# Kernel optimization log

Hardware: AMD Instinct MI355X
Metric: run time of the kernel (lower is better)

## Reference

```python
import jax, jax.numpy as jnp
import numpy as np

NUM_VNS = 16384
NUM_CNS = 8192
VN_DEG = 3
NUM_EDGES = NUM_VNS * VN_DEG  # 49152
BATCH = 128
NUM_ITER = 8
LLR_MAX = 20.0
PHI_MIN = 8.5e-8      # clip values from _phi
PHI_MAX = 16.635532


def _build_graph():
    # (3,6)-regular Tanner graph, edges listed in variable-node (column) order.
    v = np.repeat(np.arange(NUM_VNS), VN_DEG)          # vn id per edge (sorted)
    j = np.tile(np.arange(VN_DEG), NUM_VNS)
    c = (3 * v + j) % NUM_CNS                          # cn id per edge, no duplicate (v,c) pairs
    perm_cn = np.argsort(c, kind='stable')             # == ind_cn: vn-order -> cn-order
    perm_cn_inv = np.argsort(perm_cn, kind='stable')   # == ind_cn_inv
    cn_ids = c[perm_cn]                                # sorted cn id per edge (cn order)
    return (v.astype(np.int32), cn_ids.astype(np.int32),
            perm_cn.astype(np.int32), perm_cn_inv.astype(np.int32))


def setup_inputs() -> dict:
    key = jax.random.key(0)
    vn_ids, cn_ids, perm_cn, perm_cn_inv = _build_graph()
    llr_ch = 2.0 * jax.random.normal(key, (BATCH, NUM_VNS), dtype=jnp.float32)
    return {
        'llr_ch': llr_ch,
        'vn_ids': jnp.asarray(vn_ids),
        'cn_ids': jnp.asarray(cn_ids),
        'perm_cn': jnp.asarray(perm_cn),
        'perm_cn_inv': jnp.asarray(perm_cn_inv),
    }


def _phi(x):
    # numerically stable helper (Ryan), with the module's clipping
    x = jnp.clip(x, PHI_MIN, PHI_MAX)
    return jnp.log(jnp.exp(x) + 1.0) - jnp.log(jnp.exp(x) - 1.0)


def reference(llr_ch, vn_ids, cn_ids, perm_cn, perm_cn_inv):
    # internal sign convention: logits -> llrs (Sionna multiplies by -1)
    llr = -jnp.clip(llr_ch, -LLR_MAX, LLR_MAX).T       # [num_vns, batch]
    msg0 = jnp.zeros((NUM_EDGES, llr.shape[1]), llr.dtype)

    def body(msg, _):
        # --- variable node update (extrinsic): sum of incoming + channel llr, minus own ---
        vtot = jax.ops.segment_sum(msg, vn_ids, num_segments=NUM_VNS) + llr  # [num_vns, B]
        msg_vn = vtot[vn_ids] - msg                     # [num_edges, B], vn edge order
        # --- permute messages into check-node edge order ---
        m = msg_vn[perm_cn]
        # --- check node update: boxplus-phi ---
        sgn = jnp.where(m < 0, -1.0, 1.0)               # tf.sign with sign(0)->1
        sgn_node = jax.ops.segment_prod(sgn, cn_ids, num_segments=NUM_CNS)
        sgn_ext = jax.lax.stop_gradient(sgn * sgn_node[cn_ids])  # extrinsic sign (+-1)
        mag = _phi(jnp.abs(m))
        mag_sum = jax.ops.segment_sum(mag, cn_ids, num_segments=NUM_CNS)
        msg_cn = sgn_ext * _phi(mag_sum[cn_ids] - mag)  # extrinsic magnitude
        # --- back to variable-node edge order ---
        return msg_cn[perm_cn_inv], None

    msg, _ = jax.lax.scan(body, msg0, None, length=NUM_ITER)
    # marginalize: total llr per vn, then convert back to logits
    x_tot = llr + jax.ops.segment_sum(msg, vn_ids, num_segments=NUM_VNS)
    return -x_tot.T                                     # [batch, num_vns], soft output (hard_out=False)
```

## Files before the change

kernel.cpp:

```cpp
#include <hip/hip_runtime.h>


constexpr int NUM_VNS   = 16384;
constexpr int NUM_CNS   = 8192;
constexpr int NUM_EDGES = 49152;
constexpr int BATCH     = 128;
constexpr int NUM_ITER  = 8;
constexpr float LLR_MAX = 20.0f;
constexpr float PHI_MIN = 8.5e-8f;
constexpr float PHI_MAX = 16.635532f;

__device__ __forceinline__ double lean_exp(double x) {
    double t = x * 1.4426950408889634;
    double k = __builtin_rint(t);
    double r = __builtin_fma(-k, 0.6931471805599453, x);
    r = __builtin_fma(-k, 2.3190468138462996e-17, r);
    double p = 1.0 / 3628800.0;
    p = __builtin_fma(p, r, 1.0 / 362880.0);
    p = __builtin_fma(p, r, 1.0 / 40320.0);
    p = __builtin_fma(p, r, 1.0 / 5040.0);
    p = __builtin_fma(p, r, 1.0 / 720.0);
    p = __builtin_fma(p, r, 1.0 / 120.0);
    p = __builtin_fma(p, r, 1.0 / 24.0);
    p = __builtin_fma(p, r, 1.0 / 6.0);
    p = __builtin_fma(p, r, 0.5);
    p = __builtin_fma(p, r, 1.0);
    p = __builtin_fma(p, r, 1.0);
    int ik = (int)k;
    double s = __hiloint2double((1023 + ik) << 20, 0);
    return p * s;
}

__device__ __forceinline__ double lean_log(double v) {
    int hv = __double2hiint(v);
    int lv = __double2loint(v);
    int e  = (hv >> 20) - 1023;
    double m = __hiloint2double((hv & 0x000FFFFF) | 0x3FF00000, lv);
    if (m >= 1.4142135623730951) { m *= 0.5; e += 1; }
    double t = m - 1.0;
    double d = t + 2.0;
    double r = (double)__builtin_amdgcn_rcpf((float)d);
    r = __builtin_fma(__builtin_fma(-d, r, 1.0), r, r);
    double u = t * r;
    double w = u * u;
    double P = 2.0 / 13.0;
    P = __builtin_fma(P, w, 2.0 / 11.0);
    P = __builtin_fma(P, w, 2.0 / 9.0);
    P = __builtin_fma(P, w, 2.0 / 7.0);
    P = __builtin_fma(P, w, 2.0 / 5.0);
    P = __builtin_fma(P, w, 2.0 / 3.0);
    P = __builtin_fma(P, w, 2.0);
    double lm = u * P;
    return __builtin_fma((double)e, 0.6931471805599453, lm);
}

__device__ __forceinline__ float phi_f(float xf) {
    xf = fminf(fmaxf(xf, PHI_MIN), PHI_MAX);
    float exf = (float)lean_exp((double)xf);
    float af = exf + 1.0f;
    float bf = exf - 1.0f;
    float la = (float)lean_log((double)af);
    float lb = (float)lean_log((double)bf);
    return la - lb;
}

constexpr double EXP_STEP = 0.0027076061740622864;
constexpr double EXP_INV  = 369.32993046757465;

__device__ __forceinline__ double fast_exp(double x, const double* et) {
    double kd = __builtin_rint(x * EXP_INV);
    double r  = __builtin_fma(-kd, EXP_STEP, x);
    int n = (int)kd;
    double p = __builtin_fma(r, __builtin_fma(r, 0.5, 1.0), 1.0);
    double s = et[n & 255];
    int sh = __double2hiint(s) + ((n >> 8) << 20);
    s = __hiloint2double(sh, __double2loint(s));
    return p * s;
}

__device__ __forceinline__ double fast_log(double v, const double2* lt) {
    int hv = __double2hiint(v);
    int lv = __double2loint(v);
    int E  = (hv >> 20) - 1023;
    double m = __hiloint2double((hv & 0x000FFFFF) | 0x3FF00000, lv);
    int idx = (hv >> 12) & 255;
    double2 te = lt[idx];
    double t = __hiloint2double(0x3FF00000 | (idx << 12), 0);
    double d = m - t;
    double f = d * te.x;
    double P = __builtin_fma(f, 1.0 / 3.0, -0.5);
    double q = __builtin_fma(f * f, P, f);
    return __builtin_fma((double)E, 0.6931471805599453, te.y + q);
}

__device__ __forceinline__ float phi_fast(float xf, const double2* lt,
                                          const double* et) {
    xf = fminf(fmaxf(xf, PHI_MIN), PHI_MAX);
    float exf = (float)fast_exp((double)xf, et);
    float af = exf + 1.0f;
    float bf = exf - 1.0f;
    float la = (float)fast_log((double)af, lt);
    float lb = (float)fast_log((double)bf, lt);
    return la - lb;
}

template<int FIRST>
__global__ __launch_bounds__(256)
void cn_fused(const float* __restrict__ llr, const float* __restrict__ msgIn,
              float* __restrict__ msgOut)
{
    __shared__ double2 lt[256];
    __shared__ double  et[256];
    {
        int tid = threadIdx.x;
        {
            double t = 1.0 + tid * 0.00390625;
            double r0 = (double)__builtin_amdgcn_rcpf((float)t);
            r0 = __builtin_fma(__builtin_fma(-t, r0, 1.0), r0, r0);
            r0 = __builtin_fma(__builtin_fma(-t, r0, 1.0), r0, r0);
            lt[tid] = make_double2(r0, lean_log(t));
        }
        et[tid] = lean_exp(tid * EXP_STEP);
    }
    __syncthreads();

    int bid = blockIdx.x;
    int seq = bid >> 3;
    int b   = (bid & 7) * 16 + (seq >> 5);
    int c   = (seq & 31) * 256 + threadIdx.x;

    const float* mi = msgIn + (size_t)b * NUM_EDGES;
    float* mo = msgOut + (size_t)b * NUM_EDGES;
    const float* lbp = llr + (size_t)b * NUM_VNS;

    float g[6];
#pragma unroll
    for (int t = 0; t < 6; ++t) {
        int e = c + (t << 13);
        int v = (int)(((unsigned)e * 43691u) >> 17);
        float x = fminf(fmaxf(lbp[v], -LLR_MAX), LLR_MAX);
        float m;
        if (FIRST) {
            m = -x;
        } else {
            int e0 = 3 * v;
            int j  = e - e0;
            float m0 = mi[e0], m1 = mi[e0 + 1], m2 = mi[e0 + 2];
            float s = ((m0 + m1) + m2) - x;
            float own = (j == 0) ? m0 : ((j == 1) ? m1 : m2);
            m = s - own;
        }
        unsigned neg = (m < 0.0f) ? 0x80000000u : 0u;
        float mg = phi_fast(fabsf(m), lt, et);
        g[t] = __uint_as_float(__float_as_uint(mg) | neg);
    }
    float a0 = fabsf(g[0]), a1 = fabsf(g[1]), a2 = fabsf(g[2]);
    float a3 = fabsf(g[3]), a4 = fabsf(g[4]), a5 = fabsf(g[5]);
    float ms = ((((a0 + a1) + a2) + a3) + a4) + a5;
    unsigned all6 = (__float_as_uint(g[0]) ^ __float_as_uint(g[1])
                   ^ __float_as_uint(g[2]) ^ __float_as_uint(g[3])
                   ^ __float_as_uint(g[4]) ^ __float_as_uint(g[5]))
                  & 0x80000000u;
#pragma unroll
    for (int t = 0; t < 6; ++t) {
        int e = c + (t << 13);
        float o = phi_fast(ms - fabsf(g[t]), lt, et);
        unsigned sg = all6 ^ (__float_as_uint(g[t]) & 0x80000000u);
        mo[e] = __uint_as_float(__float_as_uint(o) ^ sg);
    }
}

__global__ __launch_bounds__(256)
void vn_final(const float* __restrict__ llr, const float* __restrict__ msg,
              float* __restrict__ outv)
{
    int bid = blockIdx.x;
    int seq = bid >> 3;
    int b   = (bid & 7) * 16 + (seq >> 6);
    int v   = (seq & 63) * 256 + threadIdx.x;
    float x = fminf(fmaxf(llr[(size_t)b * NUM_VNS + v], -LLR_MAX), LLR_MAX);
    const float* mb = msg + (size_t)b * NUM_EDGES;
    int e = 3 * v;
    float s = ((mb[e] + mb[e + 1]) + mb[e + 2]) - x;
    outv[(size_t)b * NUM_VNS + v] = -s;
}

template<int FIRST, int LAST>
__global__ __launch_bounds__(256)
void vn_kernel(const float* __restrict__ llr, const float* __restrict__ msg,
               float* __restrict__ outv)
{
    int gid = blockIdx.x * 256 + threadIdx.x;
    int b = gid >> 14;
    int v = gid & 16383;
    float x = fminf(fmaxf(llr[gid], -LLR_MAX), LLR_MAX);
    float s;
    if (FIRST) {
        s = -x;
    } else {
        const float* mb = msg + (size_t)b * NUM_EDGES;
        int e = 3 * v;
        s = ((mb[e] + mb[e + 1]) + mb[e + 2]) - x;
    }
    outv[gid] = LAST ? -s : s;
}

template<int FIRST>
__global__ __launch_bounds__(256)
void cn_kernel(float* __restrict__ msg, const float* __restrict__ vtot)
{
    int gid = blockIdx.x * 256 + threadIdx.x;
    int b = gid >> 13;
    int c = gid & 8191;
    float* mb = msg + (size_t)b * NUM_EDGES;
    const float* vt = vtot + (size_t)b * NUM_VNS;

    float g[6];
#pragma unroll
    for (int t = 0; t < 6; ++t) {
        int e = c + (t << 13);
        int v = (int)(((unsigned)e * 43691u) >> 17);
        float m = FIRST ? vt[v] : (vt[v] - mb[e]);
        unsigned neg = (m < 0.0f) ? 0x80000000u : 0u;
        float mg = phi_f(fabsf(m));
        g[t] = __uint_as_float(__float_as_uint(mg) | neg);
    }
    float a0 = fabsf(g[0]), a1 = fabsf(g[1]), a2 = fabsf(g[2]);
    float a3 = fabsf(g[3]), a4 = fabsf(g[4]), a5 = fabsf(g[5]);
    float ms = ((((a0 + a1) + a2) + a3) + a4) + a5;
    unsigned all6 = (__float_as_uint(g[0]) ^ __float_as_uint(g[1])
                   ^ __float_as_uint(g[2]) ^ __float_as_uint(g[3])
                   ^ __float_as_uint(g[4]) ^ __float_as_uint(g[5]))
                  & 0x80000000u;
#pragma unroll
    for (int t = 0; t < 6; ++t) {
        int e = c + (t << 13);
        float o = phi_f(ms - fabsf(g[t]));
        unsigned sg = all6 ^ (__float_as_uint(g[t]) & 0x80000000u);
        mb[e] = __uint_as_float(__float_as_uint(o) ^ sg);
    }
}

extern "C" void kernel_launch(void* const* d_in, const int* in_sizes, int n_in,
                              void* d_out, int out_size, void* d_ws, size_t ws_size,
                              hipStream_t stream) {
    const float* llr = (const float*)d_in[0];
    float* out = (float*)d_out;

    const int VNB = BATCH * NUM_VNS / 256;
    const int CNB = BATCH * NUM_CNS / 256;
    const size_t MSGSZ = (size_t)BATCH * NUM_EDGES;

    if (ws_size >= 2 * MSGSZ * sizeof(float)) {
        float* buf0 = (float*)d_ws;
        float* buf1 = buf0 + MSGSZ;
        cn_fused<1><<<CNB, 256, 0, stream>>>(llr, buf0, buf0);
        for (int it = 1; it < NUM_ITER; ++it) {
            float* in  = (it & 1) ? buf0 : buf1;
            float* dst = (it & 1) ? buf1 : buf0;
            cn_fused<0><<<CNB, 256, 0, stream>>>(llr, in, dst);
        }
        vn_final<<<VNB, 256, 0, stream>>>(llr, buf1, out);
    } else {
        float* msg  = (float*)d_ws;
        float* vtot = msg + MSGSZ;
        vn_kernel<1, 0><<<VNB, 256, 0, stream>>>(llr, msg, vtot);
        cn_kernel<1><<<CNB, 256, 0, stream>>>(msg, vtot);
        for (int it = 1; it < NUM_ITER; ++it) {
            vn_kernel<0, 0><<<VNB, 256, 0, stream>>>(llr, msg, vtot);
            cn_kernel<0><<<CNB, 256, 0, stream>>>(msg, vtot);
        }
        vn_kernel<0, 1><<<VNB, 256, 0, stream>>>(llr, msg, out);
    }
}
```

Baseline: 203.8 us.

## Fuse final VN marginalization into last CN kernel via atomics; two CNs per thread

Each thread now processes two check nodes, halving the grid so the per-block shared-memory table setup is amortized over twice the work. The last iteration's check-node kernel scatters its outgoing messages straight into the output with atomicAdd, with the channel LLR added once per variable node. This removes the separate vn_final kernel and one full message write plus read, at the cost of a memset and float atomics whose summation order is nondeterministic.

Measured after the change: 410.1 us. +101.3%, slower.

```diff
diff --git a/kernel.cpp b/kernel.cpp
--- a/kernel.cpp
+++ b/kernel.cpp
@@ -104,85 +104,86 @@
     return la - lb;
 }
 
-template<int FIRST>
+template<int FIRST, int LAST>
 __global__ __launch_bounds__(256)
-void cn_fused(const float* __restrict__ llr, const float* __restrict__ msgIn,
-              float* __restrict__ msgOut)
+void cn_fused2(const float* __restrict__ llr, const float* __restrict__ msgIn,
+               float* __restrict__ msgOut, float* __restrict__ outv)
 {
     __shared__ double2 lt[256];
     __shared__ double  et[256];
     {
         int tid = threadIdx.x;
-        {
-            double t = 1.0 + tid * 0.00390625;
-            double r0 = (double)__builtin_amdgcn_rcpf((float)t);
-            r0 = __builtin_fma(__builtin_fma(-t, r0, 1.0), r0, r0);
-            r0 = __builtin_fma(__builtin_fma(-t, r0, 1.0), r0, r0);
-            lt[tid] = make_double2(r0, lean_log(t));
-        }
+        double t = 1.0 + tid * 0.00390625;
+        double r0 = (double)__builtin_amdgcn_rcpf((float)t);
+        r0 = __builtin_fma(__builtin_fma(-t, r0, 1.0), r0, r0);
+        r0 = __builtin_fma(__builtin_fma(-t, r0, 1.0), r0, r0);
+        lt[tid] = make_double2(r0, lean_log(t));
         et[tid] = lean_exp(tid * EXP_STEP);
     }
     __syncthreads();
 
     int bid = blockIdx.x;
     int seq = bid >> 3;
-    int b   = (bid & 7) * 16 + (seq >> 5);
-    int c   = (seq & 31) * 256 + threadIdx.x;
+    int b   = (bid & 7) * 16 + (seq >> 4);
+    int ch  = (seq & 15) * 256 + threadIdx.x;
 
     const float* mi = msgIn + (size_t)b * NUM_EDGES;
     float* mo = msgOut + (size_t)b * NUM_EDGES;
     const float* lbp = llr + (size_t)b * NUM_VNS;
-
-    float g[6];
-#pragma unroll
-    for (int t = 0; t < 6; ++t) {
-        int e = c + (t << 13);
-        int v = (int)(((unsigned)e * 43691u) >> 17);
-        float x = fminf(fmaxf(lbp[v], -LLR_MAX), LLR_MAX);
-        float m;
-        if (FIRST) {
-            m = -x;
-        } else {
-            int e0 = 3 * v;
-            int j  = e - e0;
-            float m0 = mi[e0], m1 = mi[e0 + 1], m2 = mi[e0 + 2];
-            float s = ((m0 + m1) + m2) - x;
-            float own = (j == 0) ? m0 : ((j == 1) ? m1 : m2);
-            m = s - own;
-        }
-        unsigned neg = (m < 0.0f) ? 0x80000000u : 0u;
-        float mg = phi_fast(fabsf(m), lt, et);
-        g[t] = __uint_as_float(__float_as_uint(mg) | neg);
-    }
-    float a0 = fabsf(g[0]), a1 = fabsf(g[1]), a2 = fabsf(g[2]);
-    float a3 = fabsf(g[3]), a4 = fabsf(g[4]), a5 = fabsf(g[5]);
-    float ms = ((((a0 + a1) + a2) + a3) + a4) + a5;
-    unsigned all6 = (__float_as_uint(g[0]) ^ __float_as_uint(g[1])
-                   ^ __float_as_uint(g[2]) ^ __float_as_uint(g[3])
-                   ^ __float_as_uint(g[4]) ^ __float_as_uint(g[5]))
-                  & 0x80000000u;
-#pragma unroll
-    for (int t = 0; t < 6; ++t) {
-        int e = c + (t << 13);
-        float o = phi_fast(ms - fabsf(g[t]), lt, et);
-        unsigned sg = all6 ^ (__float_as_uint(g[t]) & 0x80000000u);
-        mo[e] = __uint_as_float(__float_as_uint(o) ^ sg);
-    }
-}
-
-__global__ __launch_bounds__(256)
-void vn_final(const float* __restrict__ llr, const float* __restrict__ msg,
-              float* __restrict__ outv)
-{
-    int bid = blockIdx.x;
-    int seq = bid >> 3;
-    int b   = (bid & 7) * 16 + (seq >> 6);
-    int v   = (seq & 63) * 256 + threadIdx.x;
-    float x = fminf(fmaxf(llr[(size_t)b * NUM_VNS + v], -LLR_MAX), LLR_MAX);
-    const float* mb = msg + (size_t)b * NUM_EDGES;
-    int e = 3 * v;
-    float s = ((mb[e] + mb[e + 1]) + mb[e + 2]) - x;
-    outv[(size_t)b * NUM_VNS + v] = -s;
+    float* ob = outv + (size_t)b * NUM_VNS;
+
+#pragma unroll
+    for (int h = 0; h < 2; ++h) {
+        int c = ch + (h ? 4096 : 0);
+
+        float g[6];
+#pragma unroll
+        for (int t = 0; t < 6; ++t) {
+            int e = c + (t << 13);
+            int v = (int)(((unsigned)e * 43691u) >> 17);
+            float x = fminf(fmaxf(lbp[v], -LLR_MAX), LLR_MAX);
+            float m;
+            if (FIRST) {
+                m = -x;
+            } else {
+                int e0 = 3 * v;
+                int j  = e - e0;
+                float m0 = mi[e0], m1 = mi[e0 + 1], m2 = mi[e0 + 2];
+                float s = ((m0 + m1) + m2) - x;
+                float own = (j == 0) ? m0 : ((j == 1) ? m1 : m2);
+                m = s - own;
+            }
+            unsigned neg = (m < 0.0f) ? 0x80000000u : 0u;
+            float mg = phi_fast(fabsf(m), lt, et);
+            g[t] = __uint_as_float(__float_as_uint(mg) | neg);
+        }
+        float a0 = fabsf(g[0]), a1 = fabsf(g[1]), a2 = fabsf(g[2]);
+        float a3 = fabsf(g[3]), a4 = fabsf(g[4]), a5 = fabsf(g[5]);
+        float ms = ((((a0 + a1) + a2) + a3) + a4) + a5;
+        unsigned all6 = (__float_as_uint(g[0]) ^ __float_as_uint(g[1])
+                       ^ __float_as_uint(g[2]) ^ __float_as_uint(g[3])
+                       ^ __float_as_uint(g[4]) ^ __float_as_uint(g[5]))
+                      & 0x80000000u;
+#pragma unroll
+        for (int t = 0; t < 6; ++t) {
+            int e = c + (t << 13);
+            float o = phi_fast(ms - fabsf(g[t]), lt, et);
+            unsigned sg = all6 ^ (__float_as_uint(g[t]) & 0x80000000u);
+            float osg = __uint_as_float(__float_as_uint(o) ^ sg);
+            if (LAST) {
+                int v = (int)(((unsigned)e * 43691u) >> 17);
+                int j = e - 3 * v;
+                float contrib = -osg;
+                if (j == 0) {
+                    float x = fminf(fmaxf(lbp[v], -LLR_MAX), LLR_MAX);
+                    contrib = x - osg;
+                }
+                atomicAdd(&ob[v], contrib);
+            } else {
+                mo[e] = osg;
+            }
+        }
+    }
 }
 
 template<int FIRST, int LAST>
@@ -247,20 +248,24 @@
     const float* llr = (const float*)d_in[0];
     float* out = (float*)d_out;
 
-    const int VNB = BATCH * NUM_VNS / 256;
-    const int CNB = BATCH * NUM_CNS / 256;
+    const int VNB  = BATCH * NUM_VNS / 256;
+    const int CNB  = BATCH * NUM_CNS / 256;
+    const int CNB2 = BATCH * (NUM_CNS / 2) / 256;
     const size_t MSGSZ = (size_t)BATCH * NUM_EDGES;
 
     if (ws_size >= 2 * MSGSZ * sizeof(float)) {
         float* buf0 = (float*)d_ws;
         float* buf1 = buf0 + MSGSZ;
-        cn_fused<1><<<CNB, 256, 0, stream>>>(llr, buf0, buf0);
-        for (int it = 1; it < NUM_ITER; ++it) {
+
+        hipMemsetAsync(out, 0, (size_t)out_size * sizeof(float), stream);
+
+        cn_fused2<1, 0><<<CNB2, 256, 0, stream>>>(llr, buf0, buf0, out);
+        for (int it = 1; it < NUM_ITER - 1; ++it) {
             float* in  = (it & 1) ? buf0 : buf1;
             float* dst = (it & 1) ? buf1 : buf0;
-            cn_fused<0><<<CNB, 256, 0, stream>>>(llr, in, dst);
-        }
-        vn_final<<<VNB, 256, 0, stream>>>(llr, buf1, out);
+            cn_fused2<0, 0><<<CNB2, 256, 0, stream>>>(llr, in, dst, out);
+        }
+        cn_fused2<0, 1><<<CNB2, 256, 0, stream>>>(llr, buf0, buf1, out);
     } else {
         float* msg  = (float*)d_ws;
         float* vtot = msg + MSGSZ;
```
